# Performance work log

Measured on AMD Instinct MI355X. Metric: run time of the kernel, lower is better.

The kernel has to match this reference:

```python
import jax, jax.numpy as jnp
import numpy as np

B, T, H, S, L = 1, 1024, 256, 256, 4  # batch, seq_len, hidden, state(=hidden), num_layers
EPS = 1e-5


def setup_inputs() -> dict:
    key = jax.random.key(0)
    ks = jax.random.split(key, 18)
    sc = 0.02
    return {
        "x": jax.random.normal(ks[0], (B, T, H), jnp.float32),
        "W_in": jax.random.normal(ks[1], (H, H), jnp.float32) * sc,
        "b_in": jax.random.normal(ks[2], (H,), jnp.float32) * sc,
        "W1": jax.random.normal(ks[3], (L, 2 * H, H), jnp.float32) * sc,
        "b1": jax.random.normal(ks[4], (L, 2 * H), jnp.float32) * sc,
        "W2": jax.random.normal(ks[5], (L, H, 2 * H), jnp.float32) * sc,
        "b2": jax.random.normal(ks[6], (L, H), jnp.float32) * sc,
        "gamma": jnp.ones((L, H), jnp.float32),
        "beta": jnp.zeros((L, H), jnp.float32),
        "W_dt": jax.random.normal(ks[7], (H, H), jnp.float32) * sc,
        "b_dt": jax.random.normal(ks[8], (H,), jnp.float32) * sc,
        "C": jax.random.normal(ks[9], (H, S), jnp.float32) * sc,
        "D": jnp.ones((H,), jnp.float32),
        "W_out": jax.random.normal(ks[10], (H, H), jnp.float32) * sc,
        "b_out": jax.random.normal(ks[11], (H,), jnp.float32) * sc,
    }


def _layernorm(y, g, b):
    m = y.mean(-1, keepdims=True)
    v = ((y - m) ** 2).mean(-1, keepdims=True)  # biased var, as torch LayerNorm
    return (y - m) * jax.lax.rsqrt(v + EPS) * g + b


def reference(x, W_in, b_in, W1, b1, W2, b2, gamma, beta, W_dt, b_dt, C, D, W_out, b_out):
    # input projection + residual gated-MLP stack
    h = x @ W_in.T + b_in  # (B,T,H)
    for l in range(W1.shape[0]):
        y = jax.nn.gelu(h @ W1[l].T + b1[l], approximate=False) @ W2[l].T + b2[l]
        h = _layernorm(y, gamma[l], beta[l]) + h
    dt = jax.nn.sigmoid(h @ W_dt.T + b_dt)  # (B,T,H)

    # All S rows of the state are identical (state[:,0] is a broadcast of h[:,0]
    # and each row updates identically), so the recurrence collapses to an
    # H-vector scan: v_0 = h_0 ; v_i = dt_i * v_{i-1} + (1-dt_i) * h_i.
    def step(v, inp):
        dt_i, h_i = inp  # each (B,H)
        v = dt_i * v + (1.0 - dt_i) * h_i
        return v, v

    _, vs_rest = jax.lax.scan(
        step, h[:, 0], (jnp.swapaxes(dt[:, 1:], 0, 1), jnp.swapaxes(h[:, 1:], 0, 1))
    )  # (T-1,B,H)
    vs = jnp.concatenate([h[:, :1], jnp.swapaxes(vs_rest, 0, 1)], axis=1)  # (B,T,H)

    u = vs @ C.T + D * h  # (B,T,H): C @ v_i + D*h_i, identical across state rows

    hid = h.shape[-1]  # == state_size
    # Original concatenates: step 0 contributes 1 row, each step i>0 contributes
    # S (=H) identical rows -> (B, 1+(T-1)*H, H).
    rows = jnp.concatenate([u[:, :1], jnp.repeat(u[:, 1:], hid, axis=1)], axis=1)
    return rows @ W_out.T + b_out
```

## Files before the change

### kernel.cpp

```cpp
#include <hip/hip_runtime.h>
#include <hip/hip_bf16.h>


#define T_SEQ 1024
#define H_DIM 256
#define TS 32

__device__ __forceinline__ float gelu_exact(float x) {
    return 0.5f * x * (1.0f + erff(x * 0.70710678118654752f));
}

template<int ACT>
__global__ __launch_bounds__(256) void gemm_kernel(
    const float* __restrict__ X, const float* __restrict__ W,
    const float* __restrict__ bias, float* __restrict__ Y,
    int M, int N, int K,
    const float* __restrict__ dscale, const float* __restrict__ dmat)
{
    __shared__ float Xs[TS][TS + 4];
    __shared__ float Ws[TS][TS + 4];
    const int tid = threadIdx.x;
    const int tx = tid & 15;
    const int ty = tid >> 4;
    const int n0 = blockIdx.x * TS;
    const int m0 = blockIdx.y * TS;
    const int lr = tid >> 3;
    const int lc = (tid & 7) * 4;

    float acc[2][2] = {{0.f, 0.f}, {0.f, 0.f}};

    for (int k0 = 0; k0 < K; k0 += TS) {
        const float4 xv = *reinterpret_cast<const float4*>(&X[(size_t)(m0 + lr) * K + k0 + lc]);
        const float4 wv = *reinterpret_cast<const float4*>(&W[(size_t)(n0 + lr) * K + k0 + lc]);
        *reinterpret_cast<float4*>(&Xs[lr][lc]) = xv;
        *reinterpret_cast<float4*>(&Ws[lr][lc]) = wv;
        __syncthreads();
#pragma unroll
        for (int kk = 0; kk < TS; kk += 4) {
            const float4 a0 = *reinterpret_cast<const float4*>(&Xs[ty][kk]);
            const float4 a1 = *reinterpret_cast<const float4*>(&Xs[ty + 16][kk]);
            const float4 b0 = *reinterpret_cast<const float4*>(&Ws[tx][kk]);
            const float4 b1 = *reinterpret_cast<const float4*>(&Ws[tx + 16][kk]);
            acc[0][0] = fmaf(a0.w, b0.w, fmaf(a0.z, b0.z, fmaf(a0.y, b0.y, fmaf(a0.x, b0.x, acc[0][0]))));
            acc[0][1] = fmaf(a0.w, b1.w, fmaf(a0.z, b1.z, fmaf(a0.y, b1.y, fmaf(a0.x, b1.x, acc[0][1]))));
            acc[1][0] = fmaf(a1.w, b0.w, fmaf(a1.z, b0.z, fmaf(a1.y, b0.y, fmaf(a1.x, b0.x, acc[1][0]))));
            acc[1][1] = fmaf(a1.w, b1.w, fmaf(a1.z, b1.z, fmaf(a1.y, b1.y, fmaf(a1.x, b1.x, acc[1][1]))));
        }
        __syncthreads();
    }

#pragma unroll
    for (int i = 0; i < 2; ++i)
#pragma unroll
        for (int j = 0; j < 2; ++j) {
            const int m_ = m0 + ty + 16 * i;
            const int n_ = n0 + tx + 16 * j;
            float r = acc[i][j];
            if (bias)   r += bias[n_];
            if (dscale) r += dscale[n_] * dmat[(size_t)m_ * N + n_];
            if (ACT == 1) r = gelu_exact(r);
            Y[(size_t)m_ * N + n_] = r;
        }
}

__global__ __launch_bounds__(256) void ln_residual_kernel(
    const float* __restrict__ Yin, const float* __restrict__ gamma,
    const float* __restrict__ beta, const float* __restrict__ hin,
    float* __restrict__ hout)
{
    __shared__ float red[8];
    const int row = blockIdx.x;
    const int c = threadIdx.x;
    const float y = Yin[(size_t)row * H_DIM + c];
    float s = y, s2 = y * y;
#pragma unroll
    for (int o = 1; o < 64; o <<= 1) {
        s  += __shfl_xor(s, o);
        s2 += __shfl_xor(s2, o);
    }
    const int wid = c >> 6;
    if ((c & 63) == 0) { red[wid] = s; red[4 + wid] = s2; }
    __syncthreads();
    const float ts  = red[0] + red[1] + red[2] + red[3];
    const float ts2 = red[4] + red[5] + red[6] + red[7];
    const float mean = ts * (1.0f / H_DIM);
    const float var  = ts2 * (1.0f / H_DIM) - mean * mean;
    const float inv  = rsqrtf(var + 1e-5f);
    hout[(size_t)row * H_DIM + c] =
        (y - mean) * inv * gamma[c] + beta[c] + hin[(size_t)row * H_DIM + c];
}

__global__ __launch_bounds__(1024) void scan_par(
    const float* __restrict__ dtpre, const float* __restrict__ h,
    float* __restrict__ vs)
{
    __shared__ float sA[16][64], sB[16][64];
    const int chl   = threadIdx.x & 63;
    const int chunk = threadIdx.x >> 6;
    const int c  = blockIdx.x * 64 + chl;
    const int t0 = chunk * 64;

    float A = 1.f, B = 0.f;
    for (int i = 0; i < 64; ++i) {
        const int t = t0 + i;
        const float hv = h[(size_t)t * H_DIM + c];
        float a, b;
        if (t == 0) { a = 0.f; b = hv; }
        else {
            const float dt = 1.0f / (1.0f + __expf(-dtpre[(size_t)t * H_DIM + c]));
            a = dt; b = (1.0f - dt) * hv;
        }
        A = a * A;
        B = fmaf(a, B, b);
    }
    sA[chunk][chl] = A; sB[chunk][chl] = B;
    __syncthreads();

    if (chunk == 0) {
        float pA = 1.f, pB = 0.f;
        for (int j = 0; j < 16; ++j) {
            const float cA = sA[j][chl], cB = sB[j][chl];
            sA[j][chl] = pA; sB[j][chl] = pB;
            pA = cA * pA;
            pB = fmaf(cA, pB, cB);
        }
    }
    __syncthreads();

    A = sA[chunk][chl]; B = sB[chunk][chl];
    for (int i = 0; i < 64; ++i) {
        const int t = t0 + i;
        const float hv = h[(size_t)t * H_DIM + c];
        float a, b;
        if (t == 0) { a = 0.f; b = hv; }
        else {
            const float dt = 1.0f / (1.0f + __expf(-dtpre[(size_t)t * H_DIM + c]));
            a = dt; b = (1.0f - dt) * hv;
        }
        A = a * A;
        B = fmaf(a, B, b);
        vs[(size_t)t * H_DIM + c] = B;
    }
}

__global__ __launch_bounds__(256) void replicate_f32(
    const float* __restrict__ src, float* __restrict__ out)
{
    const int i = blockIdx.x;
    const int tid = threadIdx.x;
    const int cg = tid & 63;
    const int sub = tid >> 6;

    const float4 v = *reinterpret_cast<const float4*>(&src[(size_t)i * H_DIM + cg * 4]);

    if (i == 0) {
        if (blockIdx.y == 0 && sub == 0)
            *reinterpret_cast<float4*>(&out[(size_t)cg * 4]) = v;
    } else {
        const size_t base = (size_t)(1 + (i - 1) * H_DIM + blockIdx.y * 64) * H_DIM;
#pragma unroll 4
        for (int it = 0; it < 16; ++it) {
            const size_t row_off = base + (size_t)(sub + it * 4) * H_DIM;
            *reinterpret_cast<float4*>(&out[row_off + cg * 4]) = v;
        }
    }
}

extern "C" void kernel_launch(void* const* d_in, const int* in_sizes, int n_in,
                              void* d_out, int out_size, void* d_ws, size_t ws_size,
                              hipStream_t stream)
{
    const float* x     = (const float*)d_in[0];
    const float* W_in  = (const float*)d_in[1];
    const float* b_in  = (const float*)d_in[2];
    const float* W1    = (const float*)d_in[3];
    const float* b1    = (const float*)d_in[4];
    const float* W2    = (const float*)d_in[5];
    const float* b2    = (const float*)d_in[6];
    const float* gamma = (const float*)d_in[7];
    const float* beta  = (const float*)d_in[8];
    const float* W_dt  = (const float*)d_in[9];
    const float* b_dt  = (const float*)d_in[10];
    const float* C     = (const float*)d_in[11];
    const float* D     = (const float*)d_in[12];
    const float* W_out = (const float*)d_in[13];
    const float* b_out = (const float*)d_in[14];
    float* out = (float*)d_out;

    float* ws    = (float*)d_ws;
    float* h     = ws;
    float* y1    = ws + 262144;
    float* y2    = ws + 786432;
    float* dtpre = ws + 262144;
    float* u     = ws + 524288;
    float* vs    = ws + 786432;
    float* ou    = ws + 786432;

    const dim3 blk(256);

    gemm_kernel<0><<<dim3(H_DIM / TS, T_SEQ / TS), blk, 0, stream>>>(
        x, W_in, b_in, h, T_SEQ, H_DIM, H_DIM, nullptr, nullptr);

    for (int l = 0; l < 4; ++l) {
        gemm_kernel<1><<<dim3(512 / TS, T_SEQ / TS), blk, 0, stream>>>(
            h, W1 + (size_t)l * 512 * 256, b1 + l * 512, y1,
            T_SEQ, 512, 256, nullptr, nullptr);
        gemm_kernel<0><<<dim3(H_DIM / TS, T_SEQ / TS), blk, 0, stream>>>(
            y1, W2 + (size_t)l * 256 * 512, b2 + l * 256, y2,
            T_SEQ, H_DIM, 512, nullptr, nullptr);
        ln_residual_kernel<<<dim3(T_SEQ), blk, 0, stream>>>(
            y2, gamma + l * 256, beta + l * 256, h, h);
    }

    gemm_kernel<0><<<dim3(H_DIM / TS, T_SEQ / TS), blk, 0, stream>>>(
        h, W_dt, b_dt, dtpre, T_SEQ, H_DIM, H_DIM, nullptr, nullptr);

    scan_par<<<dim3(H_DIM / 64), dim3(1024), 0, stream>>>(dtpre, h, vs);

    gemm_kernel<0><<<dim3(H_DIM / TS, T_SEQ / TS), blk, 0, stream>>>(
        vs, C, nullptr, u, T_SEQ, H_DIM, H_DIM, D, h);

    gemm_kernel<0><<<dim3(H_DIM / TS, T_SEQ / TS), blk, 0, stream>>>(
        u, W_out, b_out, ou, T_SEQ, H_DIM, H_DIM, nullptr, nullptr);

    replicate_f32<<<dim3(T_SEQ, 4), blk, 0, stream>>>(ou, out);
}
```

Measured before the change: 526.8 us.

## Replace FP32 SIMT GEMM with split-bf16 MFMA GEMM

Rewrites the shared GEMM kernel to split each fp32 operand into high and low bf16 parts and accumulate three 16x16x32 bf16 MFMA products per k-tile, emulating near-fp32 accuracy on matrix cores. Each wave computes one 16x16 sub-tile of the 32x32 block tile. This targets the scalar FMA cost of all projection and MLP GEMMs, at the price of extra conversion work, four LDS tiles, and a small loss of precision from dropping the lo*lo term.

```diff
diff --git a/kernel.cpp b/kernel.cpp
--- a/kernel.cpp
+++ b/kernel.cpp
@@ -4,63 +4,77 @@
 
 #define T_SEQ 1024
 #define H_DIM 256
-#define TS 32
+
+typedef __attribute__((ext_vector_type(8))) short short8;
+typedef __attribute__((ext_vector_type(4))) float f32x4;
 
 __device__ __forceinline__ float gelu_exact(float x) {
     return 0.5f * x * (1.0f + erff(x * 0.70710678118654752f));
 }
 
+__device__ __forceinline__ void split_bf16(float x, unsigned short& h, unsigned short& l) {
+    __hip_bfloat16 bh = __float2bfloat16(x);
+    float fh = __bfloat162float(bh);
+    __hip_bfloat16 bl = __float2bfloat16(x - fh);
+    __builtin_memcpy(&h, &bh, 2);
+    __builtin_memcpy(&l, &bl, 2);
+}
+
 template<int ACT>
-__global__ __launch_bounds__(256) void gemm_kernel(
+__global__ __launch_bounds__(256) void gemm_mfma(
     const float* __restrict__ X, const float* __restrict__ W,
     const float* __restrict__ bias, float* __restrict__ Y,
     int M, int N, int K,
     const float* __restrict__ dscale, const float* __restrict__ dmat)
 {
-    __shared__ float Xs[TS][TS + 4];
-    __shared__ float Ws[TS][TS + 4];
-    const int tid = threadIdx.x;
-    const int tx = tid & 15;
-    const int ty = tid >> 4;
-    const int n0 = blockIdx.x * TS;
-    const int m0 = blockIdx.y * TS;
-    const int lr = tid >> 3;
-    const int lc = (tid & 7) * 4;
-
-    float acc[2][2] = {{0.f, 0.f}, {0.f, 0.f}};
-
-    for (int k0 = 0; k0 < K; k0 += TS) {
+    __shared__ unsigned short Xh[32][40], Xl[32][40], Wh[32][40], Wl[32][40];
+
+    const int tid  = threadIdx.x;
+    const int lr   = tid >> 3;
+    const int lc   = (tid & 7) * 4;
+    const int wave = tid >> 6;
+    const int lane = tid & 63;
+    const int wr   = wave >> 1, wc = wave & 1;
+    const int l15  = lane & 15, ko = lane >> 4;
+    const int n0   = blockIdx.x * 32;
+    const int m0   = blockIdx.y * 32;
+
+    f32x4 acc = {0.f, 0.f, 0.f, 0.f};
+
+    for (int k0 = 0; k0 < K; k0 += 32) {
         const float4 xv = *reinterpret_cast<const float4*>(&X[(size_t)(m0 + lr) * K + k0 + lc]);
         const float4 wv = *reinterpret_cast<const float4*>(&W[(size_t)(n0 + lr) * K + k0 + lc]);
-        *reinterpret_cast<float4*>(&Xs[lr][lc]) = xv;
-        *reinterpret_cast<float4*>(&Ws[lr][lc]) = wv;
+        ushort4 xh, xl, wh, wl;
+        split_bf16(xv.x, xh.x, xl.x); split_bf16(xv.y, xh.y, xl.y);
+        split_bf16(xv.z, xh.z, xl.z); split_bf16(xv.w, xh.w, xl.w);
+        split_bf16(wv.x, wh.x, wl.x); split_bf16(wv.y, wh.y, wl.y);
+        split_bf16(wv.z, wh.z, wl.z); split_bf16(wv.w, wh.w, wl.w);
+        *reinterpret_cast<ushort4*>(&Xh[lr][lc]) = xh;
+        *reinterpret_cast<ushort4*>(&Xl[lr][lc]) = xl;
+        *reinterpret_cast<ushort4*>(&Wh[lr][lc]) = wh;
+        *reinterpret_cast<ushort4*>(&Wl[lr][lc]) = wl;
         __syncthreads();
+
+        const short8 ah = *reinterpret_cast<const short8*>(&Xh[16 * wr + l15][8 * ko]);
+        const short8 al = *reinterpret_cast<const short8*>(&Xl[16 * wr + l15][8 * ko]);
+        const short8 bh = *reinterpret_cast<const short8*>(&Wh[16 * wc + l15][8 * ko]);
+        const short8 bl = *reinterpret_cast<const short8*>(&Wl[16 * wc + l15][8 * ko]);
+        acc = __builtin_amdgcn_mfma_f32_16x16x32_bf16(ah, bh, acc, 0, 0, 0);
+        acc = __builtin_amdgcn_mfma_f32_16x16x32_bf16(ah, bl, acc, 0, 0, 0);
+        acc = __builtin_amdgcn_mfma_f32_16x16x32_bf16(al, bh, acc, 0, 0, 0);
+        __syncthreads();
+    }
+
+    const int n_ = n0 + 16 * wc + l15;
 #pragma unroll
-        for (int kk = 0; kk < TS; kk += 4) {
-            const float4 a0 = *reinterpret_cast<const float4*>(&Xs[ty][kk]);
-            const float4 a1 = *reinterpret_cast<const float4*>(&Xs[ty + 16][kk]);
-            const float4 b0 = *reinterpret_cast<const float4*>(&Ws[tx][kk]);
-            const float4 b1 = *reinterpret_cast<const float4*>(&Ws[tx + 16][kk]);
-            acc[0][0] = fmaf(a0.w, b0.w, fmaf(a0.z, b0.z, fmaf(a0.y, b0.y, fmaf(a0.x, b0.x, acc[0][0]))));
-            acc[0][1] = fmaf(a0.w, b1.w, fmaf(a0.z, b1.z, fmaf(a0.y, b1.y, fmaf(a0.x, b1.x, acc[0][1]))));
-            acc[1][0] = fmaf(a1.w, b0.w, fmaf(a1.z, b0.z, fmaf(a1.y, b0.y, fmaf(a1.x, b0.x, acc[1][0]))));
-            acc[1][1] = fmaf(a1.w, b1.w, fmaf(a1.z, b1.z, fmaf(a1.y, b1.y, fmaf(a1.x, b1.x, acc[1][1]))));
-        }
-        __syncthreads();
-    }
-
-#pragma unroll
-    for (int i = 0; i < 2; ++i)
-#pragma unroll
-        for (int j = 0; j < 2; ++j) {
-            const int m_ = m0 + ty + 16 * i;
-            const int n_ = n0 + tx + 16 * j;
-            float r = acc[i][j];
-            if (bias)   r += bias[n_];
-            if (dscale) r += dscale[n_] * dmat[(size_t)m_ * N + n_];
-            if (ACT == 1) r = gelu_exact(r);
-            Y[(size_t)m_ * N + n_] = r;
-        }
+    for (int j = 0; j < 4; ++j) {
+        const int m_ = m0 + 16 * wr + 4 * ko + j;
+        float r = acc[j];
+        if (bias)   r += bias[n_];
+        if (dscale) r += dscale[n_] * dmat[(size_t)m_ * N + n_];
+        if (ACT == 1) r = gelu_exact(r);
+        Y[(size_t)m_ * N + n_] = r;
+    }
 }
 
 __global__ __launch_bounds__(256) void ln_residual_kernel(
@@ -198,29 +212,29 @@
 
     const dim3 blk(256);
 
-    gemm_kernel<0><<<dim3(H_DIM / TS, T_SEQ / TS), blk, 0, stream>>>(
+    gemm_mfma<0><<<dim3(H_DIM / 32, T_SEQ / 32), blk, 0, stream>>>(
         x, W_in, b_in, h, T_SEQ, H_DIM, H_DIM, nullptr, nullptr);
 
     for (int l = 0; l < 4; ++l) {
-        gemm_kernel<1><<<dim3(512 / TS, T_SEQ / TS), blk, 0, stream>>>(
+        gemm_mfma<1><<<dim3(512 / 32, T_SEQ / 32), blk, 0, stream>>>(
             h, W1 + (size_t)l * 512 * 256, b1 + l * 512, y1,
             T_SEQ, 512, 256, nullptr, nullptr);
-        gemm_kernel<0><<<dim3(H_DIM / TS, T_SEQ / TS), blk, 0, stream>>>(
+        gemm_mfma<0><<<dim3(H_DIM / 32, T_SEQ / 32), blk, 0, stream>>>(
             y1, W2 + (size_t)l * 256 * 512, b2 + l * 256, y2,
             T_SEQ, H_DIM, 512, nullptr, nullptr);
         ln_residual_kernel<<<dim3(T_SEQ), blk, 0, stream>>>(
             y2, gamma + l * 256, beta + l * 256, h, h);
     }
 
-    gemm_kernel<0><<<dim3(H_DIM / TS, T_SEQ / TS), blk, 0, stream>>>(
+    gemm_mfma<0><<<dim3(H_DIM / 32, T_SEQ / 32), blk, 0, stream>>>(
         h, W_dt, b_dt, dtpre, T_SEQ, H_DIM, H_DIM, nullptr, nullptr);
 
     scan_par<<<dim3(H_DIM / 64), dim3(1024), 0, stream>>>(dtpre, h, vs);
 
-    gemm_kernel<0><<<dim3(H_DIM / TS, T_SEQ / TS), blk, 0, stream>>>(
+    gemm_mfma<0><<<dim3(H_DIM / 32, T_SEQ / 32), blk, 0, stream>>>(
         vs, C, nullptr, u, T_SEQ, H_DIM, H_DIM, D, h);
 
-    gemm_kernel<0><<<dim3(H_DIM / TS, T_SEQ / TS), blk, 0, stream>>>(
+    gemm_mfma<0><<<dim3(H_DIM / 32, T_SEQ / 32), blk, 0, stream>>>(
         u, W_out, b_out, ou, T_SEQ, H_DIM, H_DIM, nullptr, nullptr);
 
     replicate_f32<<<dim3(T_SEQ, 4), blk, 0, stream>>>(ou, out);
```

Measured after the change: 471.9 us. 1.12x faster.
